# Optimization experiments

Hardware: AMD Instinct MI355X
Metric: run time of the kernel (lower is better)

Reference implementation:

```python
import jax, jax.numpy as jnp
import numpy as np
from jax import lax

WINDOW_SIZE = 7
SIGMA = 1.5
C1 = 0.01 ** 2
C2 = 0.03 ** 2


def gaussian_window3d(window_size: int, channel: int) -> jnp.ndarray:
    g = jnp.arange(window_size, dtype=jnp.float32) - window_size // 2
    g = jnp.exp(-g ** 2 / (2.0 * SIGMA ** 2))
    g = g / g.sum()  # [k]
    w3 = g[:, None, None] * g[None, :, None] * g[None, None, :]  # [k,k,k]
    # OIDHW layout for depthwise conv: [channel, 1, k, k, k]
    return jnp.broadcast_to(w3[None, None], (channel, 1, window_size, window_size, window_size))


def depthwise_conv3d(x, window):
    # x: [N,C,D,H,W]; window: [C,1,k,k,k]; SAME padding via pad = k//2
    k = window.shape[-1]
    p = k // 2
    return lax.conv_general_dilated(
        x, window,
        window_strides=(1, 1, 1),
        padding=[(p, p)] * 3,
        dimension_numbers=('NCDHW', 'OIDHW', 'NCDHW'),
        feature_group_count=x.shape[1],
    )


def setup_inputs() -> dict:
    key = jax.random.key(0)
    k1, k2 = jax.random.split(key)
    shape = (2, 1, 160, 256, 256)
    img1 = jax.random.uniform(k1, shape, dtype=jnp.float32)
    img2 = jax.random.uniform(k2, shape, dtype=jnp.float32)
    window = gaussian_window3d(WINDOW_SIZE, shape[1])
    return {"img1": img1, "img2": img2, "window": window}


def reference(img1, img2, window):
    mu1 = depthwise_conv3d(img1, window)
    mu2 = depthwise_conv3d(img2, window)
    mu1_sq = mu1 * mu1
    mu2_sq = mu2 * mu2
    mu1_mu2 = mu1 * mu2
    sigma1_sq = depthwise_conv3d(img1 * img1, window) - mu1_sq
    sigma2_sq = depthwise_conv3d(img2 * img2, window) - mu2_sq
    sigma12 = depthwise_conv3d(img1 * img2, window) - mu1_mu2
    ssim_map = ((2.0 * mu1_mu2 + C1) * (2.0 * sigma12 + C2)) / (
        (mu1_sq + mu2_sq + C1) * (sigma1_sq + sigma2_sq + C2)
    )
    return ssim_map.mean()  # size_average=True
```

## Files before the change

kernel.cpp:

```cpp
#include <hip/hip_runtime.h>
#include <math.h>

#define HW 65536
#define DD 160
#define NB 2
#define DCH 80
#define NSL (DCH + 6)
#define NCH 2
#define TW 32
#define TH 16
#define PH 23

#define SSIM_C1 1e-4f
#define SSIM_C2 9e-4f

typedef float f32x2 __attribute__((ext_vector_type(2)));
typedef float f32x4 __attribute__((ext_vector_type(4)));

struct Gw { float g[7]; };

static __device__ __forceinline__ f32x2 s2(float v) { f32x2 r; r.x = v; r.y = v; return r; }

__global__ __launch_bounds__(256, 2) void k_fused(
    const float* __restrict__ img1, const float* __restrict__ img2,
    Gw gw, float* __restrict__ partials)
{
    __shared__ f32x2 pA[2][TW][PH];
    __shared__ f32x2 pB[2][TW][PH];
    __shared__ float pC[2][TW][PH];
    __shared__ float red[256];

    const int tid = threadIdx.x;
    const int nb = blockIdx.z >> 1;
    const int o0 = (blockIdx.z & 1) * DCH;
    const int h0 = blockIdx.y * TH;
    const int w0 = blockIdx.x * TW;
    const float* i1 = img1 + (size_t)nb * DD * HW;
    const float* i2 = img2 + (size_t)nb * DD * HW;
    const bool fastb = (blockIdx.x >= 1) && (blockIdx.x <= 6) &&
                       (blockIdx.y >= 1) && (blockIdx.y <= 14);

    const bool wth = (tid < 176);
    const int hh = tid >> 3;
    const int wb = (tid & 7) * 4;
    const int gh = h0 - 3 + hh;
    const int gwb = w0 - 3 + wb;
    const bool ghv = wth && ((unsigned)gh < 256u);
    const int ghc = gh < 0 ? 0 : (gh > 255 ? 255 : gh);
    const int gbase = gh * 256 + (gwb - 1);
    int coff[10];
    unsigned wbits = 0;
#pragma unroll
    for (int i = 0; i < 10; ++i) {
        int gwi = gwb + i;
        int gc = gwi < 0 ? 0 : (gwi > 255 ? 255 : gwi);
        coff[i] = ghc * 256 + gc;
        if (ghv && gwi == gc) wbits |= (1u << i);
    }

    const int wcol = tid & 31;
    const int hb = (tid >> 5) * 2;

    f32x2 ringA[2][7] = {};
    f32x2 ringB[2][7] = {};
    float ringC[2][7] = {};
    float lsum = 0.f;
    f32x2 cxy[10];

    auto LOAD = [&](int s) {
        const float* p1 = i1 + (size_t)s * HW;
        const float* p2 = i2 + (size_t)s * HW;
        if (fastb) {
            const f32x4 a0 = *(const f32x4*)(p1 + gbase);
            const f32x4 a1 = *(const f32x4*)(p1 + gbase + 4);
            const f32x4 a2 = *(const f32x4*)(p1 + gbase + 8);
            const f32x4 b0 = *(const f32x4*)(p2 + gbase);
            const f32x4 b1 = *(const f32x4*)(p2 + gbase + 4);
            const f32x4 b2 = *(const f32x4*)(p2 + gbase + 8);
            cxy[0].x = a0.y; cxy[1].x = a0.z; cxy[2].x = a0.w; cxy[3].x = a1.x;
            cxy[4].x = a1.y; cxy[5].x = a1.z; cxy[6].x = a1.w; cxy[7].x = a2.x;
            cxy[8].x = a2.y; cxy[9].x = a2.z;
            cxy[0].y = b0.y; cxy[1].y = b0.z; cxy[2].y = b0.w; cxy[3].y = b1.x;
            cxy[4].y = b1.y; cxy[5].y = b1.z; cxy[6].y = b1.w; cxy[7].y = b2.x;
            cxy[8].y = b2.y; cxy[9].y = b2.z;
        } else {
#pragma unroll
            for (int i = 0; i < 10; ++i) {
                const float vx = p1[coff[i]];
                const float vy = p2[coff[i]];
                const bool ok = (wbits >> i) & 1u;
                cxy[i].x = ok ? vx : 0.f;
                cxy[i].y = ok ? vy : 0.f;
            }
        }
    };

    {
        const int s0 = o0 - 3;
        if (s0 >= 0 && wth) LOAD(s0);
    }

    for (int t = 0; t < 13; ++t) {
#pragma unroll
        for (int p = 0; p < 7; ++p) {
            const int r = 7 * t + p;
            if (r <= NSL) {
                const int scur = o0 - 3 + r;
                const bool wv = (r < NSL) && (scur >= 0) && (scur < DD);
                const int snx = scur + 1;
                const bool pfv = (r + 1 < NSL) && (snx >= 0) && (snx < DD);

                if (wv && wth) {
                    f32x2 aA[4] = {};
                    f32x2 aB[4] = {};
                    float aC[4] = {};
#pragma unroll
                    for (int i = 0; i < 10; ++i) {
                        const f32x2 xi2 = cxy[i];
                        const f32x2 xx2 = xi2 * xi2;
                        const float xy = xi2.x * xi2.y;
#pragma unroll
                        for (int o = 0; o < 4; ++o) {
                            const int k = i - o;
                            if (k >= 0 && k < 7) {
                                const float gk = gw.g[k];
                                aA[o] += s2(gk) * xi2;
                                aB[o] += s2(gk) * xx2;
                                aC[o] += gk * xy;
                            }
                        }
                    }
                    const int buf = r & 1;
#pragma unroll
                    for (int o = 0; o < 4; ++o) {
                        pA[buf][wb + o][hh] = aA[o];
                        pB[buf][wb + o][hh] = aB[o];
                        pC[buf][wb + o][hh] = aC[o];
                    }
                }

                if (pfv && wth) LOAD(snx);

                if (r >= 1) {
                    const int rp = r - 1;
                    const int sp = o0 - 3 + rp;
                    const int pi = (p + 6) % 7;
                    if (sp >= 0 && sp < DD) {
                        const int buf = rp & 1;
                        f32x2 vA[8], vB[8];
                        float vC[8];
#pragma unroll
                        for (int i = 0; i < 8; ++i) {
                            vA[i] = pA[buf][wcol][hb + i];
                            vB[i] = pB[buf][wcol][hb + i];
                            vC[i] = pC[buf][wcol][hb + i];
                        }
#pragma unroll
                        for (int o = 0; o < 2; ++o) {
                            f32x2 aA = s2(0.f), aB = s2(0.f);
                            float aC = 0.f;
#pragma unroll
                            for (int k = 0; k < 7; ++k) {
                                const float gk = gw.g[k];
                                aA += s2(gk) * vA[o + k];
                                aB += s2(gk) * vB[o + k];
                                aC += gk * vC[o + k];
                            }
                            ringA[o][pi] = aA;
                            ringB[o][pi] = aB;
                            ringC[o][pi] = aC;
                        }
                    } else {
#pragma unroll
                        for (int o = 0; o < 2; ++o) {
                            ringA[o][pi] = s2(0.f);
                            ringB[o][pi] = s2(0.f);
                            ringC[o][pi] = 0.f;
                        }
                    }
                    if (r >= 7) {
                        f32x2 CA[2], CB[2];
                        float CC[2];
#pragma unroll
                        for (int o = 0; o < 2; ++o) {
                            f32x2 cA = s2(0.f), cB = s2(0.f);
                            float cC = 0.f;
#pragma unroll
                            for (int k = 0; k < 7; ++k) {
                                const float gk = gw.g[k];
                                const int pp = (pi + 1 + k) % 7;
                                cA += s2(gk) * ringA[o][pp];
                                cB += s2(gk) * ringB[o][pp];
                                cC += gk * ringC[o][pp];
                            }
                            CA[o] = cA; CB[o] = cB; CC[o] = cC;
                        }
                        f32x2 mu1, mu2, E11, E22, E12;
                        mu1.x = CA[0].x; mu1.y = CA[1].x;
                        mu2.x = CA[0].y; mu2.y = CA[1].y;
                        E11.x = CB[0].x; E11.y = CB[1].x;
                        E22.x = CB[0].y; E22.y = CB[1].y;
                        E12.x = CC[0];   E12.y = CC[1];
                        const f32x2 mu1s = mu1 * mu1;
                        const f32x2 mu2s = mu2 * mu2;
                        const f32x2 m12 = mu1 * mu2;
                        const f32x2 sg1 = E11 - mu1s;
                        const f32x2 sg2 = E22 - mu2s;
                        const f32x2 s12 = E12 - m12;
                        const f32x2 num = (s2(2.f) * m12 + s2(SSIM_C1)) *
                                          (s2(2.f) * s12 + s2(SSIM_C2));
                        const f32x2 den = (mu1s + mu2s + s2(SSIM_C1)) *
                                          (sg1 + sg2 + s2(SSIM_C2));
                        lsum += num.x * __builtin_amdgcn_rcpf(den.x)
                              + num.y * __builtin_amdgcn_rcpf(den.y);
                    }
                }
                __syncthreads();
            }
        }
    }

    red[tid] = lsum;
    __syncthreads();
    for (int off = 128; off > 0; off >>= 1) {
        if (tid < off) red[tid] += red[tid + off];
        __syncthreads();
    }
    if (tid == 0)
        partials[(blockIdx.z * gridDim.y + blockIdx.y) * gridDim.x + blockIdx.x] = red[0];
}

__global__ __launch_bounds__(256) void k_final(
    const float* __restrict__ partials, int n, float scale, float* __restrict__ out)
{
    __shared__ float red[256];
    float s = 0.f;
    for (int i = threadIdx.x; i < n; i += 256) s += partials[i];
    red[threadIdx.x] = s;
    __syncthreads();
    for (int off = 128; off > 0; off >>= 1) {
        if (threadIdx.x < off) red[threadIdx.x] += red[threadIdx.x + off];
        __syncthreads();
    }
    if (threadIdx.x == 0) out[0] = red[0] * scale;
}

extern "C" void kernel_launch(void* const* d_in, const int* in_sizes, int n_in,
                              void* d_out, int out_size, void* d_ws, size_t ws_size,
                              hipStream_t stream)
{
    const float* img1 = (const float*)d_in[0];
    const float* img2 = (const float*)d_in[1];
    float* out = (float*)d_out;
    float* partials = (float*)d_ws;

    Gw gw;
    {
        double gs[7], sum = 0.0;
        for (int i = 0; i < 7; ++i) { double x = i - 3; gs[i] = exp(-x * x / 4.5); sum += gs[i]; }
        for (int i = 0; i < 7; ++i) gw.g[i] = (float)(gs[i] / sum);
    }

    dim3 grid(256 / TW, 256 / TH, NB * NCH);
    k_fused<<<grid, dim3(256), 0, stream>>>(img1, img2, gw, partials);
    k_final<<<dim3(1), dim3(256), 0, stream>>>(
        partials, (256 / TW) * (256 / TH) * NB * NCH, (float)(1.0 / 20971520.0), out);
}
```

Measured before the change: 157.6 us.

## Split block into independent per-wave 8-wide tiles, replacing block barriers with wave barriers

Each 64-lane wave now owns its own 8x16 output tile with private LDS staging, so the per-slice __syncthreads is replaced by wave barriers and the one-slice pipelining lag between W-pass and H-pass is removed. The depth range is split into four chunks of 40 instead of two of 80, doubling the grid. The intent is to remove block-wide synchronisation stalls. The cost is more redundant halo loads (8-wide tiles need 14-wide input, 6-slice depth halo per smaller chunk) and only 44 of 64 lanes active in the load/W-pass stage.

```diff
diff --git a/kernel.cpp b/kernel.cpp
--- a/kernel.cpp
+++ b/kernel.cpp
@@ -4,12 +4,10 @@
 #define HW 65536
 #define DD 160
 #define NB 2
-#define DCH 80
+#define DCH 40
 #define NSL (DCH + 6)
-#define NCH 2
-#define TW 32
-#define TH 16
-#define PH 23
+#define NCH 4
+#define PHH 23
 
 #define SSIM_C1 1e-4f
 #define SSIM_C2 9e-4f
@@ -25,29 +23,30 @@
     const float* __restrict__ img1, const float* __restrict__ img2,
     Gw gw, float* __restrict__ partials)
 {
-    __shared__ f32x2 pA[2][TW][PH];
-    __shared__ f32x2 pB[2][TW][PH];
-    __shared__ float pC[2][TW][PH];
+    __shared__ f32x2 pA[4][8][PHH];
+    __shared__ f32x2 pB[4][8][PHH];
+    __shared__ float pC[4][8][PHH];
     __shared__ float red[256];
 
     const int tid = threadIdx.x;
-    const int nb = blockIdx.z >> 1;
-    const int o0 = (blockIdx.z & 1) * DCH;
-    const int h0 = blockIdx.y * TH;
-    const int w0 = blockIdx.x * TW;
+    const int wid = tid >> 6;
+    const int lane = tid & 63;
+    const int nb = blockIdx.z >> 2;
+    const int o0 = (blockIdx.z & 3) * DCH;
+    const int h0 = blockIdx.y * 16;
+    const int w0 = blockIdx.x * 32 + wid * 8;
     const float* i1 = img1 + (size_t)nb * DD * HW;
     const float* i2 = img2 + (size_t)nb * DD * HW;
-    const bool fastb = (blockIdx.x >= 1) && (blockIdx.x <= 6) &&
-                       (blockIdx.y >= 1) && (blockIdx.y <= 14);
-
-    const bool wth = (tid < 176);
-    const int hh = tid >> 3;
-    const int wb = (tid & 7) * 4;
-    const int gh = h0 - 3 + hh;
-    const int gwb = w0 - 3 + wb;
+
+    const bool wth = (lane < 44);
+    const int row = lane >> 1;
+    const int quad = lane & 1;
+    const int gh = h0 - 3 + row;
+    const int gwb = w0 + quad * 4 - 3;
     const bool ghv = wth && ((unsigned)gh < 256u);
+    const bool fastl = ghv && (gwb >= 1) && (gwb <= 245);
     const int ghc = gh < 0 ? 0 : (gh > 255 ? 255 : gh);
-    const int gbase = gh * 256 + (gwb - 1);
+    const int gbase = gh * 256 + gwb - 1;
     int coff[10];
     unsigned wbits = 0;
 #pragma unroll
@@ -58,8 +57,8 @@
         if (ghv && gwi == gc) wbits |= (1u << i);
     }
 
-    const int wcol = tid & 31;
-    const int hb = (tid >> 5) * 2;
+    const int wcol = lane & 7;
+    const int hb = (lane >> 3) * 2;
 
     f32x2 ringA[2][7] = {};
     f32x2 ringB[2][7] = {};
@@ -70,7 +69,7 @@
     auto LOAD = [&](int s) {
         const float* p1 = i1 + (size_t)s * HW;
         const float* p2 = i2 + (size_t)s * HW;
-        if (fastb) {
+        if (fastl) {
             const f32x4 a0 = *(const f32x4*)(p1 + gbase);
             const f32x4 a1 = *(const f32x4*)(p1 + gbase + 4);
             const f32x4 a2 = *(const f32x4*)(p1 + gbase + 8);
@@ -83,7 +82,7 @@
             cxy[0].y = b0.y; cxy[1].y = b0.z; cxy[2].y = b0.w; cxy[3].y = b1.x;
             cxy[4].y = b1.y; cxy[5].y = b1.z; cxy[6].y = b1.w; cxy[7].y = b2.x;
             cxy[8].y = b2.y; cxy[9].y = b2.z;
-        } else {
+        } else if (wth) {
 #pragma unroll
             for (int i = 0; i < 10; ++i) {
                 const float vx = p1[coff[i]];
@@ -97,16 +96,16 @@
 
     {
         const int s0 = o0 - 3;
-        if (s0 >= 0 && wth) LOAD(s0);
-    }
-
-    for (int t = 0; t < 13; ++t) {
+        if (s0 >= 0) LOAD(s0);
+    }
+
+    for (int t = 0; t < 7; ++t) {
 #pragma unroll
         for (int p = 0; p < 7; ++p) {
             const int r = 7 * t + p;
-            if (r <= NSL) {
+            if (r < NSL) {
                 const int scur = o0 - 3 + r;
-                const bool wv = (r < NSL) && (scur >= 0) && (scur < DD);
+                const bool wv = (scur >= 0 && scur < DD);
                 const int snx = scur + 1;
                 const bool pfv = (r + 1 < NSL) && (snx >= 0) && (snx < DD);
 
@@ -130,92 +129,102 @@
                             }
                         }
                     }
-                    const int buf = r & 1;
 #pragma unroll
                     for (int o = 0; o < 4; ++o) {
-                        pA[buf][wb + o][hh] = aA[o];
-                        pB[buf][wb + o][hh] = aB[o];
-                        pC[buf][wb + o][hh] = aC[o];
+                        pA[wid][quad * 4 + o][row] = aA[o];
+                        pB[wid][quad * 4 + o][row] = aB[o];
+                        pC[wid][quad * 4 + o][row] = aC[o];
                     }
                 }
-
-                if (pfv && wth) LOAD(snx);
-
-                if (r >= 1) {
-                    const int rp = r - 1;
-                    const int sp = o0 - 3 + rp;
-                    const int pi = (p + 6) % 7;
-                    if (sp >= 0 && sp < DD) {
-                        const int buf = rp & 1;
-                        f32x2 vA[8], vB[8];
-                        float vC[8];
-#pragma unroll
-                        for (int i = 0; i < 8; ++i) {
-                            vA[i] = pA[buf][wcol][hb + i];
-                            vB[i] = pB[buf][wcol][hb + i];
-                            vC[i] = pC[buf][wcol][hb + i];
-                        }
+                __builtin_amdgcn_wave_barrier();
+
+                if (pfv) LOAD(snx);
+
+                if (wv) {
+#pragma unroll
+                    for (int o = 0; o < 2; ++o) { ringA[o][p] = s2(0.f); ringB[o][p] = s2(0.f); ringC[o][p] = 0.f; }
+                    {
+                        f32x2 v[8];
+#pragma unroll
+                        for (int i = 0; i < 8; ++i) v[i] = pA[wid][wcol][hb + i];
 #pragma unroll
                         for (int o = 0; o < 2; ++o) {
-                            f32x2 aA = s2(0.f), aB = s2(0.f);
-                            float aC = 0.f;
-#pragma unroll
-                            for (int k = 0; k < 7; ++k) {
-                                const float gk = gw.g[k];
-                                aA += s2(gk) * vA[o + k];
-                                aB += s2(gk) * vB[o + k];
-                                aC += gk * vC[o + k];
-                            }
-                            ringA[o][pi] = aA;
-                            ringB[o][pi] = aB;
-                            ringC[o][pi] = aC;
-                        }
-                    } else {
+                            f32x2 a = s2(0.f);
+#pragma unroll
+                            for (int k = 0; k < 7; ++k) a += s2(gw.g[k]) * v[o + k];
+                            ringA[o][p] = a;
+                        }
+                    }
+                    {
+                        f32x2 v[8];
+#pragma unroll
+                        for (int i = 0; i < 8; ++i) v[i] = pB[wid][wcol][hb + i];
 #pragma unroll
                         for (int o = 0; o < 2; ++o) {
-                            ringA[o][pi] = s2(0.f);
-                            ringB[o][pi] = s2(0.f);
-                            ringC[o][pi] = 0.f;
-                        }
-                    }
-                    if (r >= 7) {
-                        f32x2 CA[2], CB[2];
-                        float CC[2];
+                            f32x2 a = s2(0.f);
+#pragma unroll
+                            for (int k = 0; k < 7; ++k) a += s2(gw.g[k]) * v[o + k];
+                            ringB[o][p] = a;
+                        }
+                    }
+                    {
+                        float v[8];
+#pragma unroll
+                        for (int i = 0; i < 8; ++i) v[i] = pC[wid][wcol][hb + i];
 #pragma unroll
                         for (int o = 0; o < 2; ++o) {
-                            f32x2 cA = s2(0.f), cB = s2(0.f);
-                            float cC = 0.f;
-#pragma unroll
-                            for (int k = 0; k < 7; ++k) {
-                                const float gk = gw.g[k];
-                                const int pp = (pi + 1 + k) % 7;
-                                cA += s2(gk) * ringA[o][pp];
-                                cB += s2(gk) * ringB[o][pp];
-                                cC += gk * ringC[o][pp];
-                            }
-                            CA[o] = cA; CB[o] = cB; CC[o] = cC;
-                        }
-                        f32x2 mu1, mu2, E11, E22, E12;
-                        mu1.x = CA[0].x; mu1.y = CA[1].x;
-                        mu2.x = CA[0].y; mu2.y = CA[1].y;
-                        E11.x = CB[0].x; E11.y = CB[1].x;
-                        E22.x = CB[0].y; E22.y = CB[1].y;
-                        E12.x = CC[0];   E12.y = CC[1];
-                        const f32x2 mu1s = mu1 * mu1;
-                        const f32x2 mu2s = mu2 * mu2;
-                        const f32x2 m12 = mu1 * mu2;
-                        const f32x2 sg1 = E11 - mu1s;
-                        const f32x2 sg2 = E22 - mu2s;
-                        const f32x2 s12 = E12 - m12;
-                        const f32x2 num = (s2(2.f) * m12 + s2(SSIM_C1)) *
-                                          (s2(2.f) * s12 + s2(SSIM_C2));
-                        const f32x2 den = (mu1s + mu2s + s2(SSIM_C1)) *
-                                          (sg1 + sg2 + s2(SSIM_C2));
-                        lsum += num.x * __builtin_amdgcn_rcpf(den.x)
-                              + num.y * __builtin_amdgcn_rcpf(den.y);
+                            float a = 0.f;
+#pragma unroll
+                            for (int k = 0; k < 7; ++k) a += gw.g[k] * v[o + k];
+                            ringC[o][p] = a;
+                        }
+                    }
+                } else {
+#pragma unroll
+                    for (int o = 0; o < 2; ++o) {
+                        ringA[o][p] = s2(0.f);
+                        ringB[o][p] = s2(0.f);
+                        ringC[o][p] = 0.f;
                     }
                 }
-                __syncthreads();
+                __builtin_amdgcn_wave_barrier();
+
+                if (r >= 6) {
+                    f32x2 CA[2], CB[2];
+                    float CC[2];
+#pragma unroll
+                    for (int o = 0; o < 2; ++o) {
+                        f32x2 cA = s2(0.f), cB = s2(0.f);
+                        float cC = 0.f;
+#pragma unroll
+                        for (int k = 0; k < 7; ++k) {
+                            const float gk = gw.g[k];
+                            const int pp = (p + 1 + k) % 7;
+                            cA += s2(gk) * ringA[o][pp];
+                            cB += s2(gk) * ringB[o][pp];
+                            cC += gk * ringC[o][pp];
+                        }
+                        CA[o] = cA; CB[o] = cB; CC[o] = cC;
+                    }
+                    f32x2 mu1, mu2, E11, E22, E12;
+                    mu1.x = CA[0].x; mu1.y = CA[1].x;
+                    mu2.x = CA[0].y; mu2.y = CA[1].y;
+                    E11.x = CB[0].x; E11.y = CB[1].x;
+                    E22.x = CB[0].y; E22.y = CB[1].y;
+                    E12.x = CC[0];   E12.y = CC[1];
+                    const f32x2 mu1s = mu1 * mu1;
+                    const f32x2 mu2s = mu2 * mu2;
+                    const f32x2 m12 = mu1 * mu2;
+                    const f32x2 sg1 = E11 - mu1s;
+                    const f32x2 sg2 = E22 - mu2s;
+                    const f32x2 s12 = E12 - m12;
+                    const f32x2 num = (s2(2.f) * m12 + s2(SSIM_C1)) *
+                                      (s2(2.f) * s12 + s2(SSIM_C2));
+                    const f32x2 den = (mu1s + mu2s + s2(SSIM_C1)) *
+                                      (sg1 + sg2 + s2(SSIM_C2));
+                    lsum += num.x * __builtin_amdgcn_rcpf(den.x)
+                          + num.y * __builtin_amdgcn_rcpf(den.y);
+                }
             }
         }
     }
@@ -261,8 +270,8 @@
         for (int i = 0; i < 7; ++i) gw.g[i] = (float)(gs[i] / sum);
     }
 
-    dim3 grid(256 / TW, 256 / TH, NB * NCH);
+    dim3 grid(8, 16, NB * NCH);
     k_fused<<<grid, dim3(256), 0, stream>>>(img1, img2, gw, partials);
     k_final<<<dim3(1), dim3(256), 0, stream>>>(
-        partials, (256 / TW) * (256 / TH) * NB * NCH, (float)(1.0 / 20971520.0), out);
+        partials, 8 * 16 * NB * NCH, (float)(1.0 / 20971520.0), out);
 }
```

Result: slower. 258.4 us (+64.0%).
